# Performance work log

Hardware: AMD Instinct MI355X
Metric: run time of the kernel (lower is better)

Reference implementation:

```python
import jax, jax.numpy as jnp
import numpy as np

N = 4096

def setup_inputs() -> dict:
    key = jax.random.key(0)
    kA, kB = jax.random.split(key)
    A = jnp.tril(jax.random.normal(kA, (N, N), dtype=jnp.float32))
    B = jnp.tril(jax.random.normal(kB, (N, N), dtype=jnp.float32))
    return {"A": A, "B": B}

def reference(A, B):
    # Product of two lower-triangular matrices; result is lower-triangular.
    # tril applied to the dense matmul reproduces the intended math exactly
    # (and zeroes any numerical noise in the structural-zero upper triangle).
    return jnp.tril(jnp.matmul(A, B))
```

## Files before the change

kernel.cpp:

```cpp
#include <hip/hip_runtime.h>
#include <stdint.h>

#define NN 4096
#define NB2 16
#define BK2 64

#define NHUNITS 72
#define NUNITS 172
#define TGRID 292

#define PGRID 8336

typedef __bf16 bf16x8 __attribute__((ext_vector_type(8)));
typedef float f32x4 __attribute__((ext_vector_type(4)));
typedef unsigned short ushort8 __attribute__((ext_vector_type(8)));

__device__ __forceinline__ unsigned short f2bf(float x) {
    union { float f; unsigned int u; } v; v.f = x;
    unsigned int u = v.u;
    u += 0x7fffu + ((u >> 16) & 1u);
    return (unsigned short)(u >> 16);
}

#define GLOAD16(g, l) __builtin_amdgcn_global_load_lds( \
    (const __attribute__((address_space(1))) unsigned int*)(g), \
    (__attribute__((address_space(3))) unsigned int*)(l), 16, 0, 0)

__device__ __forceinline__ void split_map(int z, int& bi, int& bj) {
    int d = 15;
    while (z >= NB2 - d) { z -= NB2 - d; --d; }
    bj = z; bi = z + d;
}

__global__ __launch_bounds__(256) void prep(const float* __restrict__ A,
                                            const float* __restrict__ B,
                                            unsigned short* __restrict__ Ab,
                                            unsigned short* __restrict__ Bt,
                                            float* __restrict__ C) {
    __shared__ float tile[64][65];
    int bid = blockIdx.x;
    int tid = threadIdx.x;

    if (bid < 4096) {
        int i = bid;
        int nslots = ((i >> 8) + 1) * 32;
        const float4* src = reinterpret_cast<const float4*>(A + (size_t)i * NN);
        unsigned short* dst = Ab + (size_t)i * NN;
        for (int p = tid; p < nslots; p += 256) {
            float4 x0 = src[p * 2], x1 = src[p * 2 + 1];
            ushort8 o;
            o[0] = f2bf(x0.x); o[1] = f2bf(x0.y); o[2] = f2bf(x0.z); o[3] = f2bf(x0.w);
            o[4] = f2bf(x1.x); o[5] = f2bf(x1.y); o[6] = f2bf(x1.z); o[7] = f2bf(x1.w);
            *reinterpret_cast<ushort8*>(dst + p * 8) = o;
        }
        return;
    }
    if (bid < 8192) {
        int s = bid - 4096;
        int n64 = s >> 6, k64 = s & 63;
        if (k64 < (n64 & ~3)) return;
        int n0 = n64 * 64, k0 = k64 * 64;
        int tx = tid & 63, ty = tid >> 6;
#pragma unroll
        for (int r = 0; r < 16; ++r) {
            int k = ty + r * 4;
            tile[k][tx] = B[(size_t)(k0 + k) * NN + n0 + tx];
        }
        __syncthreads();
#pragma unroll
        for (int r = 0; r < 16; ++r) {
            int n = ty + r * 4;
            Bt[(size_t)(n0 + n) * NN + k0 + tx] = f2bf(tile[tx][n]);
        }
        return;
    }
    {
        int zb = bid - 8192;
        int bi, bj; split_map(zb >> 2, bi, bj);
        int part = zb & 3;
        float4 zf = make_float4(0.f, 0.f, 0.f, 0.f);
        float4* cp = reinterpret_cast<float4*>(C + (size_t)(bi * 256 + part * 64) * NN + (size_t)bj * 256);
#pragma unroll
        for (int i2 = 0; i2 < 16; ++i2) {
            int slot = tid + i2 * 256;
            int row = slot >> 6, c4 = slot & 63;
            cp[(size_t)row * (NN / 4) + c4] = zf;
        }
    }
}

__global__ __launch_bounds__(512, 2) void trimm(const unsigned short* __restrict__ Ab,
                                                const unsigned short* __restrict__ Bt,
                                                float* __restrict__ C) {
    int bid = blockIdx.x;
    int tid = threadIdx.x;
    int lane = tid & 63;
    int w = tid >> 6;

    if (bid >= NUNITS) {
        int r = bid - NUNITS, bi = 0;
        while (r >= NB2 - 1 - bi) { r -= NB2 - 1 - bi; ++bi; }
        int bj = bi + 1 + r;
        float4 z = make_float4(0.f, 0.f, 0.f, 0.f);
        float4* cp = reinterpret_cast<float4*>(C + (size_t)bi * 256 * NN + (size_t)bj * 256);
#pragma unroll
        for (int i2 = 0; i2 < 32; ++i2) {
            int slot = tid + i2 * 512;
            int row = slot >> 6, c4 = slot & 63;
            cp[(size_t)row * (NN / 4) + c4] = z;
        }
        return;
    }

    int bi, bj, k_lo, k_hi;
    bool atom;
    if (bid < NHUNITS) {
        atom = true;
        int r = bid, d = 15;
        while (r >= 2 * (NB2 - d)) { r -= 2 * (NB2 - d); --d; }
        int t = r >> 1, half = r & 1;
        bj = t; bi = t + d;
        int base = bj * 256, len = (d + 1) * 128;
        k_lo = base + (half ? len : 0);
        k_hi = k_lo + len;
    } else {
        atom = false;
        int r = bid - NHUNITS, d = 7;
        while (r >= NB2 - d) { r -= NB2 - d; --d; }
        bj = r; bi = r + d;
        k_lo = bj * 256;
        k_hi = (bi + 1) * 256;
    }

    __shared__ unsigned short As[2][256 * 64];
    __shared__ unsigned short Bs[2][256 * 64];

    int wr = w >> 2;
    int wc = w & 3;

    int srow = tid >> 3;
    int sgch = (tid & 7) ^ (srow & 7);
    const unsigned short* gAs = Ab + (size_t)(bi * 256 + srow) * NN + sgch * 8;
    const unsigned short* gBs = Bt + (size_t)(bj * 256 + srow) * NN + sgch * 8;

    int fr = lane & 15;
    int ch0 = ((lane >> 4)) ^ (lane & 7);
    int ch1 = (4 | (lane >> 4)) ^ (lane & 7);

    f32x4 acc[8][4];
#pragma unroll
    for (int m = 0; m < 8; ++m)
#pragma unroll
        for (int n = 0; n < 4; ++n)
            acc[m][n] = (f32x4){0.f, 0.f, 0.f, 0.f};

    bf16x8 Aq[8], B0q[4], B1q[4];

#define STAGE(bufsel, kk) do { \
        unsigned short* la_ = &As[bufsel][0] + tid * 8; \
        unsigned short* lb_ = &Bs[bufsel][0] + tid * 8; \
        GLOAD16(gAs + (kk), la_); \
        GLOAD16(gAs + (kk) + 64 * NN, la_ + 4096); \
        GLOAD16(gAs + (kk) + 128 * NN, la_ + 8192); \
        GLOAD16(gAs + (kk) + 192 * NN, la_ + 12288); \
        GLOAD16(gBs + (kk), lb_); \
        GLOAD16(gBs + (kk) + 64 * NN, lb_ + 4096); \
        GLOAD16(gBs + (kk) + 128 * NN, lb_ + 8192); \
        GLOAD16(gBs + (kk) + 192 * NN, lb_ + 12288); \
    } while (0)

#define LDA(MH) do { \
        _Pragma("unroll") for (int m_ = 0; m_ < 4; ++m_) { \
            int row_ = wr * 128 + ((MH) * 4 + m_) * 16 + fr; \
            Aq[m_ * 2 + 0] = *reinterpret_cast<const bf16x8*>(&Ac[row_ * 64 + ch0 * 8]); \
            Aq[m_ * 2 + 1] = *reinterpret_cast<const bf16x8*>(&Ac[row_ * 64 + ch1 * 8]); \
        } \
    } while (0)

#define LDB(NH, BQ) do { \
        _Pragma("unroll") for (int n_ = 0; n_ < 2; ++n_) { \
            int row_ = wc * 64 + ((NH) * 2 + n_) * 16 + fr; \
            BQ[n_ * 2 + 0] = *reinterpret_cast<const bf16x8*>(&Bc[row_ * 64 + ch0 * 8]); \
            BQ[n_ * 2 + 1] = *reinterpret_cast<const bf16x8*>(&Bc[row_ * 64 + ch1 * 8]); \
        } \
    } while (0)

#define MFMA16(MB, NBASE, BQ) do { \
        _Pragma("unroll") for (int m_ = 0; m_ < 4; ++m_) \
        _Pragma("unroll") for (int n_ = 0; n_ < 2; ++n_) { \
            acc[(MB) + m_][(NBASE) + n_] = __builtin_amdgcn_mfma_f32_16x16x32_bf16( \
                Aq[m_ * 2 + 0], BQ[n_ * 2 + 0], acc[(MB) + m_][(NBASE) + n_], 0, 0, 0); \
            acc[(MB) + m_][(NBASE) + n_] = __builtin_amdgcn_mfma_f32_16x16x32_bf16( \
                Aq[m_ * 2 + 1], BQ[n_ * 2 + 1], acc[(MB) + m_][(NBASE) + n_], 0, 0, 0); \
        } \
    } while (0)

    int nt = (k_hi - k_lo) >> 6;

    STAGE(0, k_lo);
    __syncthreads();

    for (int t = 0; t < nt; ++t) {
        int cur = t & 1;
        const unsigned short* Ac = &As[cur][0];
        const unsigned short* Bc = &Bs[cur][0];

        LDA(0);
        LDB(0, B0q);
        if (t + 1 < nt) STAGE(cur ^ 1, k_lo + (t + 1) * BK2);
        __builtin_amdgcn_s_barrier();
        __builtin_amdgcn_s_setprio(1);
        MFMA16(0, 0, B0q);
        __builtin_amdgcn_s_setprio(0);
        __builtin_amdgcn_s_barrier();

        LDB(1, B1q);
        __builtin_amdgcn_s_barrier();
        __builtin_amdgcn_s_setprio(1);
        MFMA16(0, 2, B1q);
        __builtin_amdgcn_s_setprio(0);
        __builtin_amdgcn_s_barrier();

        LDA(1);
        __builtin_amdgcn_s_barrier();
        __builtin_amdgcn_s_setprio(1);
        MFMA16(4, 2, B1q);
        __builtin_amdgcn_s_setprio(0);
        __builtin_amdgcn_s_barrier();

        __builtin_amdgcn_s_setprio(1);
        MFMA16(4, 0, B0q);
        __builtin_amdgcn_s_setprio(0);
        __syncthreads();
    }
#undef STAGE
#undef LDA
#undef LDB
#undef MFMA16

    int crow0 = bi * 256 + wr * 128 + (lane >> 4) * 4;
    int ccol0 = bj * 256 + wc * 64 + fr;
    if (atom) {
#pragma unroll
        for (int m = 0; m < 8; ++m)
#pragma unroll
            for (int n = 0; n < 4; ++n) {
                float* cp = C + (size_t)(crow0 + m * 16) * NN + ccol0 + n * 16;
#pragma unroll
                for (int r2 = 0; r2 < 4; ++r2)
                    atomicAdd(&cp[(size_t)r2 * NN], acc[m][n][r2]);
            }
    } else {
#pragma unroll
        for (int m = 0; m < 8; ++m)
#pragma unroll
            for (int n = 0; n < 4; ++n) {
                float* cp = C + (size_t)(crow0 + m * 16) * NN + ccol0 + n * 16;
#pragma unroll
                for (int r2 = 0; r2 < 4; ++r2)
                    cp[(size_t)r2 * NN] = acc[m][n][r2];
            }
    }
}

extern "C" void kernel_launch(void* const* d_in, const int* in_sizes, int n_in,
                              void* d_out, int out_size, void* d_ws, size_t ws_size,
                              hipStream_t stream) {
    const float* A = (const float*)d_in[0];
    const float* B = (const float*)d_in[1];
    float* C = (float*)d_out;
    unsigned short* Ab = (unsigned short*)d_ws;
    unsigned short* Bt = Ab + (size_t)NN * NN;
    prep<<<PGRID, 256, 0, stream>>>(A, B, Ab, Bt, C);
    trimm<<<TGRID, 512, 0, stream>>>(Ab, Bt, C);
}
```

Before: 86.21 us.

## Rebalance split-K work units and restructure double-buffered pipeline with vmcnt waits

Replaces the fixed half-split of long diagonals with a variable split in which each tile diagonal is divided into ceil((d+1)/4) K-chunks. This evens out per-block work across 260 compute units instead of 172, at the cost of more atomic accumulation. The main loop now prefetches two stages ahead, uses an explicit vmcnt wait with one barrier pair per iteration instead of many interleaved barriers, and loads all B fragments up front. Near the end of each chunk the loop issues redundant loads (it wraps back to k_lo) to keep the vmcnt count uniform, which adds wasted memory traffic.

After: 108.6 us. 1.26x slower.

```diff
diff --git a/kernel.cpp b/kernel.cpp
--- a/kernel.cpp
+++ b/kernel.cpp
@@ -3,13 +3,12 @@
 
 #define NN 4096
 #define NB2 16
-#define BK2 64
-
-#define NHUNITS 72
-#define NUNITS 172
-#define TGRID 292
-
-#define PGRID 8336
+#define BK 64
+
+#define NUNITS 260
+#define TGRID 380
+
+#define PGRID 8504
 
 typedef __bf16 bf16x8 __attribute__((ext_vector_type(8)));
 typedef float f32x4 __attribute__((ext_vector_type(4)));
@@ -112,25 +111,26 @@
         return;
     }
 
-    int bi, bj, k_lo, k_hi;
+    int bi, bj, k_lo, nt;
     bool atom;
-    if (bid < NHUNITS) {
-        atom = true;
-        int r = bid, d = 15;
-        while (r >= 2 * (NB2 - d)) { r -= 2 * (NB2 - d); --d; }
-        int t = r >> 1, half = r & 1;
+    {
+        int r = bid, d = 15, nu;
+        for (;;) {
+            nu = (d + 4) >> 2;
+            int cnt = (NB2 - d) * nu;
+            if (r < cnt) break;
+            r -= cnt; --d;
+        }
+        int t = r / nu, part = r - t * nu;
         bj = t; bi = t + d;
-        int base = bj * 256, len = (d + 1) * 128;
-        k_lo = base + (half ? len : 0);
-        k_hi = k_lo + len;
-    } else {
-        atom = false;
-        int r = bid - NHUNITS, d = 7;
-        while (r >= NB2 - d) { r -= NB2 - d; --d; }
-        bj = r; bi = r + d;
-        k_lo = bj * 256;
-        k_hi = (bi + 1) * 256;
-    }
+        atom = (nu > 1);
+        int ntk = 4 * (d + 1);
+        int ntb = ntk / nu, rem = ntk % nu;
+        nt = ntb + (part < rem ? 1 : 0);
+        int skip = part * ntb + (part < rem ? part : rem);
+        k_lo = bj * 256 + skip * BK;
+    }
+    int k_hi = k_lo + nt * BK;
 
     __shared__ unsigned short As[2][256 * 64];
     __shared__ unsigned short Bs[2][256 * 64];
@@ -139,13 +139,9 @@
     int wc = w & 3;
 
     int srow = tid >> 3;
-    int sgch = (tid & 7) ^ (srow & 7);
-    const unsigned short* gAs = Ab + (size_t)(bi * 256 + srow) * NN + sgch * 8;
-    const unsigned short* gBs = Bt + (size_t)(bj * 256 + srow) * NN + sgch * 8;
-
-    int fr = lane & 15;
-    int ch0 = ((lane >> 4)) ^ (lane & 7);
-    int ch1 = (4 | (lane >> 4)) ^ (lane & 7);
+    int schunk = ((tid & 7) ^ (srow & 7)) * 8;
+    const unsigned short* gA = Ab + (size_t)(bi * 256 + srow) * NN + schunk;
+    const unsigned short* gB = Bt + (size_t)(bj * 256 + srow) * NN + schunk;
 
     f32x4 acc[8][4];
 #pragma unroll
@@ -154,89 +150,86 @@
         for (int n = 0; n < 4; ++n)
             acc[m][n] = (f32x4){0.f, 0.f, 0.f, 0.f};
 
-    bf16x8 Aq[8], B0q[4], B1q[4];
+    int fr = lane & 15;
+    int c0 = (((lane >> 4) ^ (lane & 7)) * 8);
+    int c1 = ((((lane >> 4) | 4) ^ (lane & 7)) * 8);
+    int arow = wr * 128 + fr;
+    int brow = wc * 64 + fr;
 
 #define STAGE(bufsel, kk) do { \
         unsigned short* la_ = &As[bufsel][0] + tid * 8; \
         unsigned short* lb_ = &Bs[bufsel][0] + tid * 8; \
-        GLOAD16(gAs + (kk), la_); \
-        GLOAD16(gAs + (kk) + 64 * NN, la_ + 4096); \
-        GLOAD16(gAs + (kk) + 128 * NN, la_ + 8192); \
-        GLOAD16(gAs + (kk) + 192 * NN, la_ + 12288); \
-        GLOAD16(gBs + (kk), lb_); \
-        GLOAD16(gBs + (kk) + 64 * NN, lb_ + 4096); \
-        GLOAD16(gBs + (kk) + 128 * NN, lb_ + 8192); \
-        GLOAD16(gBs + (kk) + 192 * NN, lb_ + 12288); \
+        GLOAD16(gA + (kk), la_); \
+        GLOAD16(gA + (kk) + (size_t)64 * NN, la_ + 4096); \
+        GLOAD16(gA + (kk) + (size_t)128 * NN, la_ + 8192); \
+        GLOAD16(gA + (kk) + (size_t)192 * NN, la_ + 12288); \
+        GLOAD16(gB + (kk), lb_); \
+        GLOAD16(gB + (kk) + (size_t)64 * NN, lb_ + 4096); \
+        GLOAD16(gB + (kk) + (size_t)128 * NN, lb_ + 8192); \
+        GLOAD16(gB + (kk) + (size_t)192 * NN, lb_ + 12288); \
     } while (0)
 
-#define LDA(MH) do { \
-        _Pragma("unroll") for (int m_ = 0; m_ < 4; ++m_) { \
-            int row_ = wr * 128 + ((MH) * 4 + m_) * 16 + fr; \
-            Aq[m_ * 2 + 0] = *reinterpret_cast<const bf16x8*>(&Ac[row_ * 64 + ch0 * 8]); \
-            Aq[m_ * 2 + 1] = *reinterpret_cast<const bf16x8*>(&Ac[row_ * 64 + ch1 * 8]); \
-        } \
-    } while (0)
-
-#define LDB(NH, BQ) do { \
-        _Pragma("unroll") for (int n_ = 0; n_ < 2; ++n_) { \
-            int row_ = wc * 64 + ((NH) * 2 + n_) * 16 + fr; \
-            BQ[n_ * 2 + 0] = *reinterpret_cast<const bf16x8*>(&Bc[row_ * 64 + ch0 * 8]); \
-            BQ[n_ * 2 + 1] = *reinterpret_cast<const bf16x8*>(&Bc[row_ * 64 + ch1 * 8]); \
-        } \
-    } while (0)
-
-#define MFMA16(MB, NBASE, BQ) do { \
-        _Pragma("unroll") for (int m_ = 0; m_ < 4; ++m_) \
-        _Pragma("unroll") for (int n_ = 0; n_ < 2; ++n_) { \
-            acc[(MB) + m_][(NBASE) + n_] = __builtin_amdgcn_mfma_f32_16x16x32_bf16( \
-                Aq[m_ * 2 + 0], BQ[n_ * 2 + 0], acc[(MB) + m_][(NBASE) + n_], 0, 0, 0); \
-            acc[(MB) + m_][(NBASE) + n_] = __builtin_amdgcn_mfma_f32_16x16x32_bf16( \
-                Aq[m_ * 2 + 1], BQ[n_ * 2 + 1], acc[(MB) + m_][(NBASE) + n_], 0, 0, 0); \
-        } \
-    } while (0)
-
-    int nt = (k_hi - k_lo) >> 6;
-
     STAGE(0, k_lo);
-    __syncthreads();
+    STAGE(1, k_lo + BK);
+    int cur = 0;
 
     for (int t = 0; t < nt; ++t) {
-        int cur = t & 1;
+        asm volatile("s_waitcnt vmcnt(8)" ::: "memory");
+        __builtin_amdgcn_s_barrier();
+
         const unsigned short* Ac = &As[cur][0];
         const unsigned short* Bc = &Bs[cur][0];
-
-        LDA(0);
-        LDB(0, B0q);
-        if (t + 1 < nt) STAGE(cur ^ 1, k_lo + (t + 1) * BK2);
+        bf16x8 b0[4], b1[4];
+#pragma unroll
+        for (int n = 0; n < 4; ++n) {
+            b0[n] = *reinterpret_cast<const bf16x8*>(&Bc[(brow + n * 16) * 64 + c0]);
+            b1[n] = *reinterpret_cast<const bf16x8*>(&Bc[(brow + n * 16) * 64 + c1]);
+        }
+        {
+            bf16x8 a0[4], a1[4];
+#pragma unroll
+            for (int m = 0; m < 4; ++m) {
+                a0[m] = *reinterpret_cast<const bf16x8*>(&Ac[(arow + m * 16) * 64 + c0]);
+                a1[m] = *reinterpret_cast<const bf16x8*>(&Ac[(arow + m * 16) * 64 + c1]);
+            }
+            __builtin_amdgcn_s_setprio(1);
+#pragma unroll
+            for (int m = 0; m < 4; ++m)
+#pragma unroll
+                for (int n = 0; n < 4; ++n) {
+                    acc[m][n] = __builtin_amdgcn_mfma_f32_16x16x32_bf16(a0[m], b0[n], acc[m][n], 0, 0, 0);
+                    acc[m][n] = __builtin_amdgcn_mfma_f32_16x16x32_bf16(a1[m], b1[n], acc[m][n], 0, 0, 0);
+                }
+            __builtin_amdgcn_s_setprio(0);
+        }
+        {
+            bf16x8 a0[4], a1[4];
+#pragma unroll
+            for (int m = 0; m < 4; ++m) {
+                a0[m] = *reinterpret_cast<const bf16x8*>(&Ac[(arow + 64 + m * 16) * 64 + c0]);
+                a1[m] = *reinterpret_cast<const bf16x8*>(&Ac[(arow + 64 + m * 16) * 64 + c1]);
+            }
+            __builtin_amdgcn_s_setprio(1);
+#pragma unroll
+            for (int m = 0; m < 4; ++m)
+#pragma unroll
+                for (int n = 0; n < 4; ++n) {
+                    acc[m + 4][n] = __builtin_amdgcn_mfma_f32_16x16x32_bf16(a0[m], b0[n], acc[m + 4][n], 0, 0, 0);
+                    acc[m + 4][n] = __builtin_amdgcn_mfma_f32_16x16x32_bf16(a1[m], b1[n], acc[m + 4][n], 0, 0, 0);
+                }
+            __builtin_amdgcn_s_setprio(0);
+        }
+
         __builtin_amdgcn_s_barrier();
-        __builtin_amdgcn_s_setprio(1);
-        MFMA16(0, 0, B0q);
-        __builtin_amdgcn_s_setprio(0);
-        __builtin_amdgcn_s_barrier();
-
-        LDB(1, B1q);
-        __builtin_amdgcn_s_barrier();
-        __builtin_amdgcn_s_setprio(1);
-        MFMA16(0, 2, B1q);
-        __builtin_amdgcn_s_setprio(0);
-        __builtin_amdgcn_s_barrier();
-
-        LDA(1);
-        __builtin_amdgcn_s_barrier();
-        __builtin_amdgcn_s_setprio(1);
-        MFMA16(4, 2, B1q);
-        __builtin_amdgcn_s_setprio(0);
-        __builtin_amdgcn_s_barrier();
-
-        __builtin_amdgcn_s_setprio(1);
-        MFMA16(4, 0, B0q);
-        __builtin_amdgcn_s_setprio(0);
-        __syncthreads();
-    }
+
+        int kn = k_lo + (t + 2) * BK;
+        if (kn >= k_hi) kn = k_lo;
+        STAGE(cur, kn);
+
+        cur ^= 1;
+    }
+    asm volatile("s_waitcnt vmcnt(0)" ::: "memory");
 #undef STAGE
-#undef LDA
-#undef LDB
-#undef MFMA16
 
     int crow0 = bi * 256 + wr * 128 + (lane >> 4) * 4;
     int ccol0 = bj * 256 + wc * 64 + fr;
```
